# Kernel optimization log

Hardware: AMD Instinct MI355X
Metric: run time of the kernel (lower is better)

Reference implementation:

```python
import jax, jax.numpy as jnp
import numpy as np

DT = 0.01
G = 9.81
M = 1.5
E3 = jnp.array([0.0, 0.0, 1.0], dtype=jnp.float32)
K = 8388608


def setup_inputs() -> dict:
    key = jax.random.key(0)
    k1, k2, k3 = jax.random.split(key, 3)
    f = jax.random.normal(k1, (K, 3), dtype=jnp.float32)
    p_0 = jax.random.normal(k2, (3,), dtype=jnp.float32)
    v_0 = jax.random.normal(k3, (3,), dtype=jnp.float32)
    return {"f": f, "p_0": p_0, "v_0": v_0}


def reference(f, p_0, v_0):
    K_ = f.shape[0]
    # Original loop: v[0] uses f[0]; v[i+1] uses f[i]  =>  f index per step: [0, 0, 1, ..., K-2]
    idx = jnp.concatenate([jnp.zeros(1, dtype=jnp.int32), jnp.arange(K_ - 1, dtype=jnp.int32)])
    a = (DT / M) * f[idx] - (DT * G) * E3          # [K,3] per-step velocity increment
    v = v_0[None, :] + jnp.cumsum(a, axis=0)       # [K,3]
    v_prev = jnp.concatenate([v_0[None, :], v[:-1]], axis=0)
    p = p_0[None, :] + (DT / 2) * jnp.cumsum(v + v_prev, axis=0)  # trapezoidal position
    return (p, v)
```

## Files before the change

kernel.cpp:

```cpp
#include <hip/hip_runtime.h>


namespace {
constexpr int  KE    = 8388608;
constexpr int  CHUNK = 2048;
constexpr int  NB    = KE / CHUNK;
constexpr int  BLOCK = 256;
constexpr int  R     = CHUNK / BLOCK;
constexpr int  NF4   = 3 * CHUNK / 4;
constexpr int  PRET  = 1024;
constexpr int  BPT   = NB / PRET;
constexpr float DTc = 0.01f;
constexpr float Cc  = 0.01f / 1.5f;
constexpr float GZ  = -0.01f * 9.81f;
typedef float f32x4 __attribute__((ext_vector_type(4)));
__device__ __forceinline__ int physf4(int q) { return 7 * (q / 6) + q % 6; }
}

__global__ __launch_bounds__(BLOCK) void k_agg(const float* __restrict__ f,
                                               float* __restrict__ W) {
  const int b = blockIdx.x, t = threadIdx.x;
  const int lane = t & 63, wid = t >> 6;
  const f32x4* src = (const f32x4*)(f + (size_t)3 * CHUNK * b);
  float A[3] = {0.f, 0.f, 0.f}, Bw[3] = {0.f, 0.f, 0.f};
#pragma unroll
  for (int it = 0; it < 2; ++it) {
    int q3 = it * BLOCK + t;
    f32x4 d0 = src[3 * q3], d1 = src[3 * q3 + 1], d2 = src[3 * q3 + 2];
    float j0 = (float)(4 * q3), j1 = j0 + 1.f, j2 = j0 + 2.f, j3 = j0 + 3.f;
    A[0] += d0.x; Bw[0] += j0 * d0.x;  A[1] += d0.y; Bw[1] += j0 * d0.y;  A[2] += d0.z; Bw[2] += j0 * d0.z;
    A[0] += d0.w; Bw[0] += j1 * d0.w;  A[1] += d1.x; Bw[1] += j1 * d1.x;  A[2] += d1.y; Bw[2] += j1 * d1.y;
    A[0] += d1.z; Bw[0] += j2 * d1.z;  A[1] += d1.w; Bw[1] += j2 * d1.w;  A[2] += d2.x; Bw[2] += j2 * d2.x;
    A[0] += d2.y; Bw[0] += j3 * d2.y;  A[1] += d2.z; Bw[1] += j3 * d2.z;  A[2] += d2.w; Bw[2] += j3 * d2.w;
  }
#pragma unroll
  for (int d = 32; d >= 1; d >>= 1) {
#pragma unroll
    for (int q = 0; q < 3; ++q) {
      A[q]  += __shfl_down(A[q], d);
      Bw[q] += __shfl_down(Bw[q], d);
    }
  }
  __shared__ float wag[4][6];
  if (lane == 0) {
#pragma unroll
    for (int q = 0; q < 3; ++q) { wag[wid][q] = A[q]; wag[wid][3 + q] = Bw[q]; }
  }
  __syncthreads();
  if (t == 0) {
#pragma unroll
    for (int q = 0; q < 3; ++q) {
      W[q * NB + b]       = wag[0][q] + wag[1][q] + wag[2][q] + wag[3][q];
      W[(3 + q) * NB + b] = wag[0][3 + q] + wag[1][3 + q] + wag[2][3 + q] + wag[3][3 + q];
    }
  }
}

__global__ __launch_bounds__(PRET) void k_pre(const float* __restrict__ W,
                                              float* __restrict__ W2) {
  const int t = threadIdx.x, lane = t & 63, wid = t >> 6;
  double Ac[BPT][3], Wc[BPT][3];
#pragma unroll
  for (int k = 0; k < BPT; ++k) {
    const int c = BPT * t + k;
#pragma unroll
    for (int q = 0; q < 3; ++q) {
      double a  = (double)W[q * NB + c];
      double bw = (double)W[(3 + q) * NB + c];
      Ac[k][q] = a;
      Wc[k][q] = (double)(CHUNK - 1) * a - bw;
    }
  }
  double tA[3] = {0, 0, 0}, tW[3] = {0, 0, 0};
#pragma unroll
  for (int k = 0; k < BPT; ++k) {
#pragma unroll
    for (int q = 0; q < 3; ++q) {
      tW[q] += (double)((BPT - 1 - k) * CHUNK) * Ac[k][q] + Wc[k][q];
      tA[q] += Ac[k][q];
    }
  }
#pragma unroll
  for (int d = 1; d < 64; d <<= 1) {
    double pA[3], pW[3];
#pragma unroll
    for (int q = 0; q < 3; ++q) { pA[q] = __shfl_up(tA[q], d); pW[q] = __shfl_up(tW[q], d); }
    if (lane >= d) {
      const double Ld = (double)(d * BPT * CHUNK);
#pragma unroll
      for (int q = 0; q < 3; ++q) { tW[q] = pW[q] + Ld * pA[q] + tW[q]; tA[q] += pA[q]; }
    }
  }
  double eA[3], eW[3];
#pragma unroll
  for (int q = 0; q < 3; ++q) { eA[q] = __shfl_up(tA[q], 1); eW[q] = __shfl_up(tW[q], 1); }
  if (lane == 0) {
#pragma unroll
    for (int q = 0; q < 3; ++q) { eA[q] = 0.0; eW[q] = 0.0; }
  }
  __shared__ double wagd[16][6];
  if (lane == 63) {
#pragma unroll
    for (int q = 0; q < 3; ++q) { wagd[wid][q] = tA[q]; wagd[wid][3 + q] = tW[q]; }
  }
  __syncthreads();
  double oA[3] = {0, 0, 0}, oW[3] = {0, 0, 0};
  for (int w = 0; w < wid; ++w) {
#pragma unroll
    for (int q = 0; q < 3; ++q) oW[q] = oW[q] + (double)(64 * BPT * CHUNK) * oA[q] + wagd[w][3 + q];
#pragma unroll
    for (int q = 0; q < 3; ++q) oA[q] += wagd[w][q];
  }
  double Ex[3], Hx[3];
#pragma unroll
  for (int q = 0; q < 3; ++q) {
    Ex[q] = oA[q] + eA[q];
    Hx[q] = oW[q] + (double)(lane * BPT * CHUNK) * oA[q] + eW[q];
  }
#pragma unroll
  for (int k = 0; k < BPT; ++k) {
    const int c = BPT * t + k;
#pragma unroll
    for (int q = 0; q < 3; ++q) {
      W2[6 * c + q]     = (float)Ex[q];
      W2[6 * c + 3 + q] = (float)Hx[q];
      Hx[q] += (double)CHUNK * Ex[q] + Wc[k][q];
      Ex[q] += Ac[k][q];
    }
  }
}

__global__ __launch_bounds__(BLOCK, 5) void k_scan(const float* __restrict__ f,
                                                   const float* __restrict__ W2,
                                                   const float* __restrict__ p0v,
                                                   const float* __restrict__ v0v,
                                                   float* __restrict__ out) {
  const int b = blockIdx.x, t = threadIdx.x;
  const int lane = t & 63, wid = t >> 6;
  const long start = (long)b * CHUNK;

  float Wg[6];
#pragma unroll
  for (int u = 0; u < 6; ++u) Wg[u] = W2[6 * b + u];
  const float f0[3] = {f[0], f[1], f[2]};
  const float p0x = p0v[0], p0y = p0v[1], p0z = p0v[2];
  const float v0x = v0v[0], v0y = v0v[1], v0z = v0v[2];

  __shared__ f32x4 buf[7 * BLOCK];
  __shared__ float wag[4][6];

  {
    const f32x4* src = (const f32x4*)(f + 3 * start);
#pragma unroll
    for (int it = 0; it < 6; ++it) {
      const int q = t + BLOCK * it;
      buf[physf4(q)] = src[q];
    }
  }
  __syncthreads();

  float z[3 * R];
#pragma unroll
  for (int u = 0; u < 6; ++u) {
    f32x4 d = buf[7 * t + u];
    z[4 * u] = d.x; z[4 * u + 1] = d.y; z[4 * u + 2] = d.z; z[4 * u + 3] = d.w;
  }

  float tS[3] = {0, 0, 0}, tT[3] = {0, 0, 0};
#pragma unroll
  for (int e = 0; e < R; ++e) {
    const float wt = (float)(R - 1 - e);
#pragma unroll
    for (int q = 0; q < 3; ++q) { float v = z[3 * e + q]; tS[q] += v; tT[q] += wt * v; }
  }
#pragma unroll
  for (int d = 1; d < 64; d <<= 1) {
    float pS[3], pT[3];
#pragma unroll
    for (int q = 0; q < 3; ++q) { pS[q] = __shfl_up(tS[q], d); pT[q] = __shfl_up(tT[q], d); }
    if (lane >= d) {
      const float Ld = (float)(R * d);
#pragma unroll
      for (int q = 0; q < 3; ++q) { tT[q] = pT[q] + Ld * pS[q] + tT[q]; tS[q] += pS[q]; }
    }
  }
  float eS[3], eT[3];
#pragma unroll
  for (int q = 0; q < 3; ++q) { eS[q] = __shfl_up(tS[q], 1); eT[q] = __shfl_up(tT[q], 1); }
  if (lane == 0) {
#pragma unroll
    for (int q = 0; q < 3; ++q) { eS[q] = 0.f; eT[q] = 0.f; }
  }
  if (lane == 63) {
#pragma unroll
    for (int q = 0; q < 3; ++q) { wag[wid][q] = tS[q]; wag[wid][3 + q] = tT[q]; }
  }
  __syncthreads();
  float oS[3] = {0, 0, 0}, oT[3] = {0, 0, 0};
  for (int w = 0; w < wid; ++w) {
#pragma unroll
    for (int q = 0; q < 3; ++q) oT[q] = oT[q] + 512.0f * oS[q] + wag[w][3 + q];
#pragma unroll
    for (int q = 0; q < 3; ++q) oS[q] += wag[w][q];
  }
  float E0[3], H0[3];
#pragma unroll
  for (int q = 0; q < 3; ++q) {
    E0[q] = Wg[q] + oS[q] + eS[q];
    H0[q] = Wg[3 + q] + (float)(R * t) * Wg[q] + (oT[q] + (float)(R * lane) * oS[q] + eT[q]);
  }

  const float a1 = DTc * Cc, a2 = 0.5f * DTc * Cc, c3 = 0.5f * DTc * GZ;
  float lsum[3] = {0, 0, 0};
  float runH[3] = {H0[0], H0[1], H0[2]};
  float ve[3 * R];
#pragma unroll
  for (int g = 0; g < 2; ++g) {
    float pe[12];
#pragma unroll
    for (int e4 = 0; e4 < 4; ++e4) {
      const int e = 4 * g + e4;
      const float n1 = (float)(int)(start + t * R + e + 1);
      float S_[3], T_[3];
#pragma unroll
      for (int q = 0; q < 3; ++q) {
        const float curE = E0[q] + lsum[q];
        runH[q] += curE;
        S_[q] = f0[q] + curE;
        T_[q] = n1 * f0[q] + runH[q];
        lsum[q] += z[3 * e + q];
      }
      ve[3 * e + 0] = v0x + Cc * S_[0];
      ve[3 * e + 1] = v0y + Cc * S_[1];
      ve[3 * e + 2] = v0z + Cc * S_[2] + GZ * n1;
      pe[3 * e4 + 0] = p0x + DTc * n1 * v0x + a1 * T_[0] - a2 * S_[0];
      pe[3 * e4 + 1] = p0y + DTc * n1 * v0y + a1 * T_[1] - a2 * S_[1];
      pe[3 * e4 + 2] = p0z + DTc * n1 * v0z + a1 * T_[2] - a2 * S_[2] + c3 * n1 * n1;
    }
#pragma unroll
    for (int u = 0; u < 3; ++u) {
      f32x4 pv = {pe[4 * u], pe[4 * u + 1], pe[4 * u + 2], pe[4 * u + 3]};
      buf[7 * t + 3 * g + u] = pv;
    }
  }

  asm volatile("s_waitcnt lgkmcnt(0)" ::: "memory");
  {
    f32x4* dst = (f32x4*)out + (size_t)NF4 * b + 384 * wid;
#pragma unroll
    for (int it = 0; it < 6; ++it) {
      const int j = it * 64 + lane;
      f32x4 d = buf[448 * wid + physf4(j)];
      __builtin_nontemporal_store(d, dst + j);
    }
  }

  asm volatile("s_waitcnt lgkmcnt(0)" ::: "memory");
#pragma unroll
  for (int u = 0; u < 6; ++u) {
    f32x4 vv = {ve[4 * u], ve[4 * u + 1], ve[4 * u + 2], ve[4 * u + 3]};
    buf[7 * t + u] = vv;
  }
  asm volatile("s_waitcnt lgkmcnt(0)" ::: "memory");
  {
    f32x4* dst = (f32x4*)(out + (size_t)3 * KE) + (size_t)NF4 * b + 384 * wid;
#pragma unroll
    for (int it = 0; it < 6; ++it) {
      const int j = it * 64 + lane;
      f32x4 d = buf[448 * wid + physf4(j)];
      __builtin_nontemporal_store(d, dst + j);
    }
  }
}

extern "C" void kernel_launch(void* const* d_in, const int* in_sizes, int n_in,
                              void* d_out, int out_size, void* d_ws, size_t ws_size,
                              hipStream_t stream) {
  const float* f  = (const float*)d_in[0];
  const float* p0 = (const float*)d_in[1];
  const float* v0 = (const float*)d_in[2];
  float* out = (float*)d_out;
  float* W   = (float*)d_ws;
  float* W2  = W + 6 * NB;
  k_agg <<<NB, BLOCK, 0, stream>>>(f, W);
  k_pre <<<1, PRET, 0, stream>>>(W, W2);
  k_scan<<<NB, BLOCK, 0, stream>>>(f, W2, p0, v0, out);
}
```

Before: 75.38 us.

## Fold single-block prefix kernel into scan blocks via redundant per-block reduction

```diff
diff --git a/kernel.cpp b/kernel.cpp
--- a/kernel.cpp
+++ b/kernel.cpp
@@ -8,8 +8,7 @@
 constexpr int  BLOCK = 256;
 constexpr int  R     = CHUNK / BLOCK;
 constexpr int  NF4   = 3 * CHUNK / 4;
-constexpr int  PRET  = 1024;
-constexpr int  BPT   = NB / PRET;
+constexpr int  CPT   = NB / BLOCK;
 constexpr float DTc = 0.01f;
 constexpr float Cc  = 0.01f / 1.5f;
 constexpr float GZ  = -0.01f * 9.81f;
@@ -56,82 +55,8 @@
   }
 }
 
-__global__ __launch_bounds__(PRET) void k_pre(const float* __restrict__ W,
-                                              float* __restrict__ W2) {
-  const int t = threadIdx.x, lane = t & 63, wid = t >> 6;
-  double Ac[BPT][3], Wc[BPT][3];
-#pragma unroll
-  for (int k = 0; k < BPT; ++k) {
-    const int c = BPT * t + k;
-#pragma unroll
-    for (int q = 0; q < 3; ++q) {
-      double a  = (double)W[q * NB + c];
-      double bw = (double)W[(3 + q) * NB + c];
-      Ac[k][q] = a;
-      Wc[k][q] = (double)(CHUNK - 1) * a - bw;
-    }
-  }
-  double tA[3] = {0, 0, 0}, tW[3] = {0, 0, 0};
-#pragma unroll
-  for (int k = 0; k < BPT; ++k) {
-#pragma unroll
-    for (int q = 0; q < 3; ++q) {
-      tW[q] += (double)((BPT - 1 - k) * CHUNK) * Ac[k][q] + Wc[k][q];
-      tA[q] += Ac[k][q];
-    }
-  }
-#pragma unroll
-  for (int d = 1; d < 64; d <<= 1) {
-    double pA[3], pW[3];
-#pragma unroll
-    for (int q = 0; q < 3; ++q) { pA[q] = __shfl_up(tA[q], d); pW[q] = __shfl_up(tW[q], d); }
-    if (lane >= d) {
-      const double Ld = (double)(d * BPT * CHUNK);
-#pragma unroll
-      for (int q = 0; q < 3; ++q) { tW[q] = pW[q] + Ld * pA[q] + tW[q]; tA[q] += pA[q]; }
-    }
-  }
-  double eA[3], eW[3];
-#pragma unroll
-  for (int q = 0; q < 3; ++q) { eA[q] = __shfl_up(tA[q], 1); eW[q] = __shfl_up(tW[q], 1); }
-  if (lane == 0) {
-#pragma unroll
-    for (int q = 0; q < 3; ++q) { eA[q] = 0.0; eW[q] = 0.0; }
-  }
-  __shared__ double wagd[16][6];
-  if (lane == 63) {
-#pragma unroll
-    for (int q = 0; q < 3; ++q) { wagd[wid][q] = tA[q]; wagd[wid][3 + q] = tW[q]; }
-  }
-  __syncthreads();
-  double oA[3] = {0, 0, 0}, oW[3] = {0, 0, 0};
-  for (int w = 0; w < wid; ++w) {
-#pragma unroll
-    for (int q = 0; q < 3; ++q) oW[q] = oW[q] + (double)(64 * BPT * CHUNK) * oA[q] + wagd[w][3 + q];
-#pragma unroll
-    for (int q = 0; q < 3; ++q) oA[q] += wagd[w][q];
-  }
-  double Ex[3], Hx[3];
-#pragma unroll
-  for (int q = 0; q < 3; ++q) {
-    Ex[q] = oA[q] + eA[q];
-    Hx[q] = oW[q] + (double)(lane * BPT * CHUNK) * oA[q] + eW[q];
-  }
-#pragma unroll
-  for (int k = 0; k < BPT; ++k) {
-    const int c = BPT * t + k;
-#pragma unroll
-    for (int q = 0; q < 3; ++q) {
-      W2[6 * c + q]     = (float)Ex[q];
-      W2[6 * c + 3 + q] = (float)Hx[q];
-      Hx[q] += (double)CHUNK * Ex[q] + Wc[k][q];
-      Ex[q] += Ac[k][q];
-    }
-  }
-}
-
 __global__ __launch_bounds__(BLOCK, 5) void k_scan(const float* __restrict__ f,
-                                                   const float* __restrict__ W2,
+                                                   const float* __restrict__ W,
                                                    const float* __restrict__ p0v,
                                                    const float* __restrict__ v0v,
                                                    float* __restrict__ out) {
@@ -139,15 +64,13 @@
   const int lane = t & 63, wid = t >> 6;
   const long start = (long)b * CHUNK;
 
-  float Wg[6];
-#pragma unroll
-  for (int u = 0; u < 6; ++u) Wg[u] = W2[6 * b + u];
   const float f0[3] = {f[0], f[1], f[2]};
   const float p0x = p0v[0], p0y = p0v[1], p0z = p0v[2];
   const float v0x = v0v[0], v0y = v0v[1], v0z = v0v[2];
 
   __shared__ f32x4 buf[7 * BLOCK];
   __shared__ float wag[4][6];
+  __shared__ float pag[4][6];
 
   {
     const f32x4* src = (const f32x4*)(f + 3 * start);
@@ -157,7 +80,40 @@
       buf[physf4(q)] = src[q];
     }
   }
+
+  float Ea[3] = {0.f, 0.f, 0.f}, Ha[3] = {0.f, 0.f, 0.f};
+#pragma unroll
+  for (int k = 0; k < CPT; ++k) {
+    const int c = t + BLOCK * k;
+    const bool sel = (c < b);
+    const float ws = sel ? ((float)(b - 1 - c) * 2048.f + 2047.f) : 0.f;
+#pragma unroll
+    for (int q = 0; q < 3; ++q) {
+      const float a  = W[q * NB + c];
+      const float bw = W[(3 + q) * NB + c];
+      Ea[q] += sel ? a : 0.f;
+      Ha[q] += ws * a - (sel ? bw : 0.f);
+    }
+  }
+#pragma unroll
+  for (int d = 32; d >= 1; d >>= 1) {
+#pragma unroll
+    for (int q = 0; q < 3; ++q) {
+      Ea[q] += __shfl_down(Ea[q], d);
+      Ha[q] += __shfl_down(Ha[q], d);
+    }
+  }
+  if (lane == 0) {
+#pragma unroll
+    for (int q = 0; q < 3; ++q) { pag[wid][q] = Ea[q]; pag[wid][3 + q] = Ha[q]; }
+  }
   __syncthreads();
+  float Eg[3], Hg[3];
+#pragma unroll
+  for (int q = 0; q < 3; ++q) {
+    Eg[q] = pag[0][q] + pag[1][q] + pag[2][q] + pag[3][q];
+    Hg[q] = pag[0][3 + q] + pag[1][3 + q] + pag[2][3 + q] + pag[3][3 + q];
+  }
 
   float z[3 * R];
 #pragma unroll
@@ -206,8 +162,8 @@
   float E0[3], H0[3];
 #pragma unroll
   for (int q = 0; q < 3; ++q) {
-    E0[q] = Wg[q] + oS[q] + eS[q];
-    H0[q] = Wg[3 + q] + (float)(R * t) * Wg[q] + (oT[q] + (float)(R * lane) * oS[q] + eT[q]);
+    E0[q] = Eg[q] + oS[q] + eS[q];
+    H0[q] = Hg[q] + (float)(R * t) * Eg[q] + (oT[q] + (float)(R * lane) * oS[q] + eT[q]);
   }
 
   const float a1 = DTc * Cc, a2 = 0.5f * DTc * Cc, c3 = 0.5f * DTc * GZ;
@@ -281,8 +237,6 @@
   const float* v0 = (const float*)d_in[2];
   float* out = (float*)d_out;
   float* W   = (float*)d_ws;
-  float* W2  = W + 6 * NB;
   k_agg <<<NB, BLOCK, 0, stream>>>(f, W);
-  k_pre <<<1, PRET, 0, stream>>>(W, W2);
-  k_scan<<<NB, BLOCK, 0, stream>>>(f, W2, p0, v0, out);
-}
+  k_scan<<<NB, BLOCK, 0, stream>>>(f, W, p0, v0, out);
+}
```

New measurement: 69.18 us. -8.2%, faster.
